# Kernel tuning notes

Measured on AMD Instinct MI355X. Metric: run time of the kernel, lower is better.

Reference implementation:

```python
import jax, jax.numpy as jnp
import numpy as np

N_NODES = 50000
N_EDGES = 600000
N_GRAPHS = 2048
EMB = 128
N_LAYERS = 3
ATOM_FEATS, ATOM_VOCAB = 9, 100
BOND_FEATS, BOND_VOCAB, BOND_DIM = 3, 8, 3


def setup_inputs() -> dict:
    key = jax.random.key(0)
    ks = jax.random.split(key, 10)
    x = jax.random.randint(ks[0], (N_NODES, ATOM_FEATS), 0, ATOM_VOCAB)
    edge_index = jax.random.randint(ks[1], (2, N_EDGES), 0, N_NODES)
    edge_attr = jax.random.randint(ks[2], (N_EDGES, BOND_FEATS), 0, BOND_VOCAB)
    batch = jnp.sort(jax.random.randint(ks[3], (N_NODES,), 0, N_GRAPHS))
    s = 1.0 / np.sqrt(EMB).astype(np.float32)
    atom_emb = jax.random.normal(ks[4], (ATOM_FEATS, ATOM_VOCAB, EMB), jnp.float32) * 0.1
    bond_emb = jax.random.normal(ks[5], (N_LAYERS, BOND_FEATS, BOND_VOCAB, BOND_DIM), jnp.float32) * 0.1
    W = jax.random.normal(ks[6], (N_LAYERS, BOND_DIM, EMB, EMB), jnp.float32) * s
    b = jnp.zeros((N_LAYERS, BOND_DIM, EMB), jnp.float32)
    fc1_w = jax.random.normal(ks[7], (EMB, EMB), jnp.float32) * s
    fc1_b = jnp.zeros((EMB,), jnp.float32)
    fc2_w = jax.random.normal(ks[8], (EMB, 1), jnp.float32) * s
    fc2_b = jnp.zeros((1,), jnp.float32)
    return dict(x=x, edge_index=edge_index, edge_attr=edge_attr, batch=batch,
                atom_emb=atom_emb, bond_emb=bond_emb, W=W, b=b,
                fc1_w=fc1_w, fc1_b=fc1_b, fc2_w=fc2_w, fc2_b=fc2_b)


def reference(x, edge_index, edge_attr, batch, atom_emb, bond_emb, W, b,
              fc1_w, fc1_b, fc2_w, fc2_b):
    src, dst = edge_index[0], edge_index[1]
    n = x.shape[0]
    # AtomEncoder: sum of per-column embedding lookups -> [N, EMB]
    h = atom_emb[0][x[:, 0]]
    for c in range(1, ATOM_FEATS):
        h = h + atom_emb[c][x[:, c]]
    for layer in range(N_LAYERS):
        # BondEncoder: [E, BOND_DIM] edge weights (one scalar channel per conv)
        ew = bond_emb[layer, 0][edge_attr[:, 0]]
        for c in range(1, BOND_FEATS):
            ew = ew + bond_emb[layer, c][edge_attr[:, c]]
        # Three parallel GCNConv(normalize=False): linear, gather src, edge-weight, scatter-add to dst
        msg = jnp.zeros((edge_index.shape[1], EMB), h.dtype)
        for k in range(BOND_DIM):
            xw = h @ W[layer, k]              # [N, EMB]
            msg = msg + ew[:, k:k + 1] * xw[src]   # [E, EMB]
        agg = jax.ops.segment_sum(msg, dst, num_segments=n)
        hn = agg + jnp.sum(b[layer], axis=0)  # sum of the three conv biases
        if layer < N_LAYERS - 1:
            hn = jax.nn.relu(hn)              # dropout is identity at eval
        h = hn + h                            # residual
    # global_mean_pool
    sums = jax.ops.segment_sum(h, batch, num_segments=N_GRAPHS)
    counts = jax.ops.segment_sum(jnp.ones((n,), h.dtype), batch, num_segments=N_GRAPHS)
    hg = sums / jnp.maximum(counts, 1.0)[:, None]
    return (hg @ fc1_w + fc1_b) @ fc2_w + fc2_b   # [N_GRAPHS, 1]
```

## Files before the change

### kernel.cpp

```cpp
#include <hip/hip_runtime.h>

#define N_NODES 50000
#define N_EDGES 600000
#define N_GRAPHS 2048
#define EMB 128
#define TDIM 384
#define TS_LD 392
#define HN (N_NODES * EMB)
#define GROWS 64

#define EPB 2048
#define NBLKA ((N_EDGES + EPB - 1) / EPB)
#define NCOARSE ((N_NODES + 255) / 256)
#define SCAN_TOT (NCOARSE * NBLKA)
#define SC2_NB ((SCAN_TOT + 255) / 256)

#define PRE_CNT_NB NBLKA
#define PRE_WCONV_NB 384
#define PRE_GB_NB 131

#define ATOM_HALF 25000
#define ATOM_NB 6250

typedef __attribute__((ext_vector_type(8))) short bf16x8;
typedef __attribute__((ext_vector_type(4))) float f32x4;
#define MFMA_BF16(a, b, c) __builtin_amdgcn_mfma_f32_16x16x32_bf16(a, b, c, 0, 0, 0)

#define AS1 __attribute__((address_space(1)))
#define AS3 __attribute__((address_space(3)))
__device__ inline void gl_lds16(const void* g, void* l) {
  __builtin_amdgcn_global_load_lds((const AS1 void*)g, (AS3 void*)l, 16, 0, 0);
}

__device__ inline unsigned short f2bf(float f) {
  unsigned int u = __float_as_uint(f);
  u += 0x7fffu + ((u >> 16) & 1u);
  return (unsigned short)(u >> 16);
}
__device__ inline float bf2f(unsigned short b) {
  return __uint_as_float(((unsigned int)b) << 16);
}
__device__ inline bf16x8 pack8(float4 lo, float4 hi) {
  bf16x8 r;
  r[0] = (short)f2bf(lo.x); r[1] = (short)f2bf(lo.y);
  r[2] = (short)f2bf(lo.z); r[3] = (short)f2bf(lo.w);
  r[4] = (short)f2bf(hi.x); r[5] = (short)f2bf(hi.y);
  r[6] = (short)f2bf(hi.z); r[7] = (short)f2bf(hi.w);
  return r;
}

__device__ inline void atom_block(int nbase, int blk, const int* __restrict__ x,
                                  const float* __restrict__ atom_emb,
                                  unsigned short* __restrict__ h_bf, float* sb) {
  const int wv = threadIdx.x >> 6;
  const int lane = threadIdx.x & 63;
  int n = nbase + blk * 4 + wv;
  if (n < N_NODES) {
    const int nu = __builtin_amdgcn_readfirstlane(n);
    const int* xr = x + nu * 9;
    int ix[9];
#pragma unroll
    for (int c = 0; c < 9; ++c) ix[c] = xr[c];
    float* wbase = sb + wv * 1280;
    const int half = lane >> 5;
    const int sub16 = lane & 31;
#pragma unroll
    for (int j = 0; j < 4; ++j) {
      int c = 2 * j + half;
      const float* g = atom_emb + (size_t)(c * 100 + ix[c]) * EMB + sub16 * 4;
      gl_lds16(g, wbase + j * 256);
    }
    {
      const float* g = atom_emb + (size_t)(8 * 100 + ix[8]) * EMB + sub16 * 4;
      gl_lds16(g, wbase + 1024);
    }
    asm volatile("s_waitcnt vmcnt(0)" ::: "memory");
    float2 acc = {0.f, 0.f};
#pragma unroll
    for (int c = 0; c < 9; ++c) {
      float2 v = *(const float2*)(wbase + c * 128 + lane * 2);
      acc.x += v.x; acc.y += v.y;
    }
    *(ushort2*)(h_bf + (size_t)nu * EMB + lane * 2) = ushort2{f2bf(acc.x), f2bf(acc.y)};
  }
}

__global__ __launch_bounds__(384) void k_pre(const int* __restrict__ ei,
                                             int* __restrict__ ghist,
                                             const float* __restrict__ W,
                                             unsigned short* __restrict__ wt,
                                             const int* __restrict__ batch,
                                             int* __restrict__ gs) {
  __shared__ int h[256];
  int blk = blockIdx.x;
  if (blk < PRE_CNT_NB) {
    const int t = threadIdx.x;
    if (t < 256) h[t] = 0;
    __syncthreads();
    const int base = blk * EPB;
#pragma unroll
    for (int k = 0; k < 6; ++k) {
      int o = k * 384 + t;
      int e = base + o;
      if (o < EPB && e < N_EDGES) atomicAdd(&h[ei[N_EDGES + e] >> 8], 1);
    }
    __syncthreads();
    if (t < NCOARSE) ghist[(size_t)t * NBLKA + blk] = h[t];
    return;
  }
  blk -= PRE_CNT_NB;
  if (blk < PRE_WCONV_NB) {
    int layer = blk >> 7, c = blk & 127, k = threadIdx.x;
    float v = W[(((layer * 3 + (k >> 7)) * 128) + (k & 127)) * 128 + c];
    wt[(size_t)blk * 384 + k] = f2bf(v);
    return;
  }
  blk -= PRE_WCONV_NB;
  {
    int i = blk * 384 + threadIdx.x;
    if (i < N_NODES) {
      int b = batch[i];
      int bp = (i == 0) ? -1 : batch[i - 1];
      for (int g = bp + 1; g <= b; ++g) gs[g] = i;
      if (i == N_NODES - 1) {
        for (int g = b + 1; g <= N_GRAPHS; ++g) gs[g] = N_NODES;
      }
    }
  }
}

__global__ __launch_bounds__(256) void k_gscan_a(int* __restrict__ ghist,
                                                 int* __restrict__ partials) {
  __shared__ int s[256];
  const int t = threadIdx.x;
  const int i = blockIdx.x * 256 + t;
  int v = (i < SCAN_TOT) ? ghist[i] : 0;
  s[t] = v;
  __syncthreads();
  for (int off = 1; off < 256; off <<= 1) {
    int u = (t >= off) ? s[t - off] : 0;
    __syncthreads();
    s[t] += u;
    __syncthreads();
  }
  if (i < SCAN_TOT) ghist[i] = s[t] - v;
  if (t == 255) partials[blockIdx.x] = s[255];
}

__global__ __launch_bounds__(256) void k_gscan_b(int* __restrict__ partials,
                                                 int* __restrict__ bucket_base,
                                                 int* __restrict__ row_start) {
  __shared__ int s[256];
  const int t = threadIdx.x;
  int v = (t < SC2_NB) ? partials[t] : 0;
  s[t] = v;
  __syncthreads();
  for (int off = 1; off < 256; off <<= 1) {
    int u = (t >= off) ? s[t - off] : 0;
    __syncthreads();
    s[t] += u;
    __syncthreads();
  }
  if (t < SC2_NB) partials[t] = s[t] - v;
  if (t == 0) { bucket_base[NCOARSE] = N_EDGES; row_start[N_NODES] = N_EDGES; }
}

__global__ __launch_bounds__(256) void k_gscan_c(int* __restrict__ ghist,
                                                 const int* __restrict__ partials,
                                                 int* __restrict__ bucket_base) {
  const int i = blockIdx.x * 256 + threadIdx.x;
  if (i < SCAN_TOT) {
    int g = ghist[i] + partials[blockIdx.x];
    ghist[i] = g;
    int d = i / NBLKA;
    if (i - d * NBLKA == 0) bucket_base[d] = g;
  }
}

__global__ __launch_bounds__(256) void k_coarse(const int* __restrict__ ei,
                                                const int* __restrict__ ea,
                                                const int* __restrict__ ghist,
                                                int2* __restrict__ tmp,
                                                const int* __restrict__ x,
                                                const float* __restrict__ atom_emb,
                                                unsigned short* __restrict__ h_bf) {
  __shared__ float sb[4 * 1280];
  if (blockIdx.x >= NBLKA) {
    atom_block(0, blockIdx.x - NBLKA, x, atom_emb, h_bf, sb);
    return;
  }
  int* cnt = (int*)sb;
  const int t = threadIdx.x;
  cnt[t] = 0;
  __syncthreads();
  const int base = blockIdx.x * EPB;
#pragma unroll
  for (int k = 0; k < 8; ++k) {
    int e = base + k * 256 + t;
    if (e < N_EDGES) {
      int dst = ei[N_EDGES + e];
      int d = dst >> 8;
      int r = atomicAdd(&cnt[d], 1);
      int pos = ghist[(size_t)d * NBLKA + blockIdx.x] + r;
      int eap = ea[e * 3 + 0] | (ea[e * 3 + 1] << 3) | (ea[e * 3 + 2] << 6);
      tmp[pos] = int2{dst | (eap << 16), ei[e]};
    }
  }
}

__global__ __launch_bounds__(256) void k_fine(const int2* __restrict__ tmp,
                                              const int* __restrict__ bucket_base,
                                              int* __restrict__ row_start,
                                              int2* __restrict__ sorted_se,
                                              const int* __restrict__ x,
                                              const float* __restrict__ atom_emb,
                                              unsigned short* __restrict__ h_bf) {
  __shared__ float sb[4 * 1280];
  if (blockIdx.x >= NCOARSE) {
    atom_block(ATOM_HALF, blockIdx.x - NCOARSE, x, atom_emb, h_bf, sb);
    return;
  }
  int* h = (int*)sb;
  int* s = h + 256;
  int* ex = s + 256;
  const int t = threadIdx.x;
  const int d = blockIdx.x;
  const int b0 = bucket_base[d], b1 = bucket_base[d + 1];
  h[t] = 0;
  __syncthreads();
  for (int i = b0 + t; i < b1; i += 256) atomicAdd(&h[tmp[i].x & 255], 1);
  __syncthreads();
  s[t] = h[t];
  __syncthreads();
  for (int off = 1; off < 256; off <<= 1) {
    int v = (t >= off) ? s[t - off] : 0;
    __syncthreads();
    s[t] += v;
    __syncthreads();
  }
  ex[t] = s[t] - h[t];
  int node = d * 256 + t;
  if (node < N_NODES) row_start[node] = b0 + ex[t];
  h[t] = 0;
  __syncthreads();
  for (int i = b0 + t; i < b1; i += 256) {
    int2 r = tmp[i];
    int f = r.x & 255;
    int pos = b0 + ex[f] + atomicAdd(&h[f], 1);
    sorted_se[pos] = int2{r.y, (r.x >> 16) & 511};
  }
}

__global__ __launch_bounds__(256) void k_agg(const int2* __restrict__ sorted_se,
                                             const int* __restrict__ row_start,
                                             const float* __restrict__ bl,
                                             const unsigned short* __restrict__ h_bf,
                                             unsigned short* __restrict__ t_bf) {
  __shared__ float4 combo[512];
  const int node = blockIdx.x * 16 + (threadIdx.x >> 4);
  const int sub = threadIdx.x & 15;
  const int beg = row_start[node], end = row_start[node + 1];
  int e = beg;
  const int full_end = beg + ((end - beg) & ~7);
  int2 se[8];
  if (e < full_end) {
#pragma unroll
    for (int j = 0; j < 8; ++j) se[j] = sorted_se[e + j];
  }
  for (int c = threadIdx.x; c < 512; c += 256) {
    int a0 = c & 7, a1 = (c >> 3) & 7, a2 = (c >> 6) & 7;
    combo[c] = float4{bl[a0 * 3 + 0] + bl[24 + a1 * 3 + 0] + bl[48 + a2 * 3 + 0],
                      bl[a0 * 3 + 1] + bl[24 + a1 * 3 + 1] + bl[48 + a2 * 3 + 1],
                      bl[a0 * 3 + 2] + bl[24 + a1 * 3 + 2] + bl[48 + a2 * 3 + 2], 0.f};
  }
  __syncthreads();
  float4 l0 = {0.f, 0.f, 0.f, 0.f}, h0 = l0;
  float4 l1 = l0, h1 = l0;
  float4 l2 = l0, h2 = l0;
  while (e < full_end) {
    bf16x8 u[8];
#pragma unroll
    for (int j = 0; j < 8; ++j)
      u[j] = *(const bf16x8*)(h_bf + (size_t)se[j].x * EMB + sub * 8);
    e += 8;
    int2 se_n[8];
    const bool more = (e < full_end);
    if (more) {
#pragma unroll
      for (int j = 0; j < 8; ++j) se_n[j] = sorted_se[e + j];
    }
#pragma unroll
    for (int j = 0; j < 8; ++j) {
      float4 w = combo[se[j].y];
      float4 vlo = {bf2f((unsigned short)u[j][0]), bf2f((unsigned short)u[j][1]),
                    bf2f((unsigned short)u[j][2]), bf2f((unsigned short)u[j][3])};
      float4 vhi = {bf2f((unsigned short)u[j][4]), bf2f((unsigned short)u[j][5]),
                    bf2f((unsigned short)u[j][6]), bf2f((unsigned short)u[j][7])};
      l0 += vlo * w.x; h0 += vhi * w.x;
      l1 += vlo * w.y; h1 += vhi * w.y;
      l2 += vlo * w.z; h2 += vhi * w.z;
    }
    if (more) {
#pragma unroll
      for (int j = 0; j < 8; ++j) se[j] = se_n[j];
    }
  }
  if (e < end) {
    int2 st[8];
#pragma unroll
    for (int j = 0; j < 8; ++j) {
      int idx = e + j;
      st[j] = sorted_se[idx < end ? idx : end - 1];
    }
    bf16x8 u[8];
#pragma unroll
    for (int j = 0; j < 8; ++j)
      u[j] = *(const bf16x8*)(h_bf + (size_t)st[j].x * EMB + sub * 8);
#pragma unroll
    for (int j = 0; j < 8; ++j) {
      float4 w = (e + j < end) ? combo[st[j].y] : float4{0.f, 0.f, 0.f, 0.f};
      float4 vlo = {bf2f((unsigned short)u[j][0]), bf2f((unsigned short)u[j][1]),
                    bf2f((unsigned short)u[j][2]), bf2f((unsigned short)u[j][3])};
      float4 vhi = {bf2f((unsigned short)u[j][4]), bf2f((unsigned short)u[j][5]),
                    bf2f((unsigned short)u[j][6]), bf2f((unsigned short)u[j][7])};
      l0 += vlo * w.x; h0 += vhi * w.x;
      l1 += vlo * w.y; h1 += vhi * w.y;
      l2 += vlo * w.z; h2 += vhi * w.z;
    }
  }
  size_t base = (size_t)node * TDIM + sub * 8;
  *(bf16x8*)(t_bf + base)       = pack8(l0, h0);
  *(bf16x8*)(t_bf + base + 128) = pack8(l1, h1);
  *(bf16x8*)(t_bf + base + 256) = pack8(l2, h2);
}

__global__ __launch_bounds__(512) void k_gemm(const unsigned short* __restrict__ t_bf,
                                              const unsigned short* __restrict__ wt,
                                              const float* __restrict__ bl,
                                              const unsigned short* __restrict__ h_in_bf,
                                              unsigned short* __restrict__ h_out_bf,
                                              int do_relu) {
  __shared__ unsigned short ts[GROWS * TS_LD];
  const int nb = blockIdx.x * GROWS;
  const int wv = threadIdx.x >> 6;
  const int lane = threadIdx.x & 63;
  const int m = lane & 15;
  const int kq = lane >> 4;
  const int c = wv * 16 + m;

  const unsigned short* pB = wt + (size_t)c * TDIM + kq * 8;
  bf16x8 B[12];
#pragma unroll
  for (int kc = 0; kc < 12; ++kc) B[kc] = *(const bf16x8*)(pB + kc * 32);
  const float bias = bl[c] + bl[128 + c] + bl[256 + c];

  for (int i = threadIdx.x; i < GROWS * 48; i += 512) {
    int r = i / 48, cc = i % 48;
    bf16x8 v = {};
    int row = nb + r;
    if (row < N_NODES) v = *(const bf16x8*)(t_bf + (size_t)row * TDIM + cc * 8);
    *(bf16x8*)(ts + r * TS_LD + cc * 8) = v;
  }
  __syncthreads();

#pragma unroll
  for (int rt = 0; rt < 4; ++rt) {
    const unsigned short* pA = ts + (rt * 16 + m) * TS_LD + kq * 8;
    bf16x8 A[12];
#pragma unroll
    for (int kc = 0; kc < 12; ++kc) A[kc] = *(const bf16x8*)(pA + kc * 32);
    f32x4 acc = {0.f, 0.f, 0.f, 0.f};
#pragma unroll
    for (int kc = 0; kc < 12; ++kc) acc = MFMA_BF16(A[kc], B[kc], acc);
#pragma unroll
    for (int r = 0; r < 4; ++r) {
      int row = nb + rt * 16 + kq * 4 + r;
      if (row < N_NODES) {
        size_t idx = (size_t)row * EMB + c;
        float v = acc[r] + bias;
        if (do_relu) v = fmaxf(v, 0.f);
        float hn = bf2f(h_in_bf[idx]) + v;
        h_out_bf[idx] = f2bf(hn);
      }
    }
  }
}

__global__ __launch_bounds__(128) void k_head(const unsigned short* __restrict__ h_bf,
                                              const int* __restrict__ gs,
                                              const float* __restrict__ fc1_w,
                                              const float* __restrict__ fc1_b,
                                              const float* __restrict__ fc2_w,
                                              const float* __restrict__ fc2_b,
                                              float* __restrict__ out) {
  __shared__ float hg[EMB];
  __shared__ float red[EMB];
  int g = blockIdx.x, e = threadIdx.x;
  int ns = gs[g], ne = gs[g + 1];
  float acc = 0.f;
  for (int n = ns; n < ne; ++n) acc += bf2f(h_bf[(size_t)n * EMB + e]);
  float cnt = fmaxf((float)(ne - ns), 1.f);
  hg[e] = acc / cnt;
  __syncthreads();
  float a2 = fc1_b[e];
  for (int j = 0; j < EMB; ++j) a2 += hg[j] * fc1_w[j * EMB + e];
  red[e] = a2 * fc2_w[e];
  __syncthreads();
  for (int s = 64; s > 0; s >>= 1) {
    if (e < s) red[e] += red[e + s];
    __syncthreads();
  }
  if (e == 0) out[g] = red[0] + fc2_b[0];
}

extern "C" void kernel_launch(void* const* d_in, const int* in_sizes, int n_in,
                              void* d_out, int out_size, void* d_ws, size_t ws_size,
                              hipStream_t stream) {
  const int*   x        = (const int*)d_in[0];
  const int*   ei       = (const int*)d_in[1];
  const int*   ea       = (const int*)d_in[2];
  const int*   batch    = (const int*)d_in[3];
  const float* atom_emb = (const float*)d_in[4];
  const float* bond_emb = (const float*)d_in[5];
  const float* W        = (const float*)d_in[6];
  const float* b        = (const float*)d_in[7];
  const float* fc1_w    = (const float*)d_in[8];
  const float* fc1_b    = (const float*)d_in[9];
  const float* fc2_w    = (const float*)d_in[10];
  const float* fc2_b    = (const float*)d_in[11];
  float* out = (float*)d_out;

  char* p = (char*)d_ws;
  auto alloc = [&](size_t bytes) { char* r = p; p += (bytes + 255) & ~(size_t)255; return r; };
  unsigned short* h0_bf      = (unsigned short*)alloc((size_t)HN * 2);
  unsigned short* h1_bf      = (unsigned short*)alloc((size_t)HN * 2);
  unsigned short* t_bf       = (unsigned short*)alloc((size_t)N_NODES * TDIM * 2);
  unsigned short* wt         = (unsigned short*)alloc((size_t)3 * 128 * TDIM * 2);
  int*            gs         = (int*)alloc((size_t)(N_GRAPHS + 1) * 4);
  int*            row_start  = (int*)alloc((size_t)(N_NODES + 1) * 4);
  int*            ghist      = (int*)alloc((size_t)SCAN_TOT * 4);
  int*            spart      = (int*)alloc((size_t)SC2_NB * 4);
  int*            bucket_base= (int*)alloc((size_t)(NCOARSE + 1) * 4);
  int2*           tmp_se     = (int2*)alloc((size_t)N_EDGES * 8);
  int2*           sorted_se  = (int2*)alloc((size_t)(N_EDGES + 8) * 8);

  const int pre_blocks = PRE_CNT_NB + PRE_WCONV_NB + PRE_GB_NB;
  k_pre<<<pre_blocks, 384, 0, stream>>>(ei, ghist, W, wt, batch, gs);
  k_gscan_a<<<SC2_NB, 256, 0, stream>>>(ghist, spart);
  k_gscan_b<<<1, 256, 0, stream>>>(spart, bucket_base, row_start);
  k_gscan_c<<<SC2_NB, 256, 0, stream>>>(ghist, spart, bucket_base);
  k_coarse<<<NBLKA + ATOM_NB, 256, 0, stream>>>(ei, ea, ghist, tmp_se,
                                                x, atom_emb, h0_bf);
  k_fine<<<NCOARSE + ATOM_NB, 256, 0, stream>>>(tmp_se, bucket_base, row_start, sorted_se,
                                                x, atom_emb, h0_bf);

  unsigned short* hib = h0_bf;
  unsigned short* hob = h1_bf;
  const int gemm_blocks = (N_NODES + GROWS - 1) / GROWS;
  for (int layer = 0; layer < 3; ++layer) {
    k_agg<<<N_NODES / 16, 256, 0, stream>>>(sorted_se, row_start, bond_emb + layer * 72,
                                            hib, t_bf);
    k_gemm<<<gemm_blocks, 512, 0, stream>>>(
        t_bf, wt + (size_t)layer * 128 * TDIM, b + layer * 3 * EMB,
        hib, hob, layer < 2 ? 1 : 0);
    unsigned short* tb = hib; hib = hob; hob = tb;
  }

  k_head<<<N_GRAPHS, 128, 0, stream>>>(hib, gs, fc1_w, fc1_b, fc2_w, fc2_b, out);
}
```

Before: 304.3 us.

## Fuse edge aggregation and GEMM into one per-layer kernel with LDS accumulation

Merges the aggregation kernel and the MFMA GEMM kernel into a single per-layer kernel, so the [N,384] bf16 intermediate tensor is no longer written to and read back from global memory. Each block takes 32 destination nodes and splits their edge range evenly across 32 groups of 16 threads for load balance. Each group accumulates partial sums in registers and flushes them into an fp32 LDS tile with atomicAdd whenever the destination node changes. The destination node index is now packed into the sorted edge record. The trade-off is LDS atomic traffic, a larger LDS footprint that may cut occupancy, and smaller 32-row GEMM tiles that reload the weight fragments more often.

```diff
diff --git a/kernel.cpp b/kernel.cpp
--- a/kernel.cpp
+++ b/kernel.cpp
@@ -7,7 +7,10 @@
 #define TDIM 384
 #define TS_LD 392
 #define HN (N_NODES * EMB)
-#define GROWS 64
+
+#define FN 32
+#define FGRID ((N_NODES + FN - 1) / FN)
+#define ACC_LD 388
 
 #define EPB 2048
 #define NBLKA ((N_EDGES + EPB - 1) / EPB)
@@ -39,14 +42,6 @@
 }
 __device__ inline float bf2f(unsigned short b) {
   return __uint_as_float(((unsigned int)b) << 16);
-}
-__device__ inline bf16x8 pack8(float4 lo, float4 hi) {
-  bf16x8 r;
-  r[0] = (short)f2bf(lo.x); r[1] = (short)f2bf(lo.y);
-  r[2] = (short)f2bf(lo.z); r[3] = (short)f2bf(lo.w);
-  r[4] = (short)f2bf(hi.x); r[5] = (short)f2bf(hi.y);
-  r[6] = (short)f2bf(hi.z); r[7] = (short)f2bf(hi.w);
-  return r;
 }
 
 __device__ inline void atom_block(int nbase, int blk, const int* __restrict__ x,
@@ -247,51 +242,83 @@
     int2 r = tmp[i];
     int f = r.x & 255;
     int pos = b0 + ex[f] + atomicAdd(&h[f], 1);
-    sorted_se[pos] = int2{r.y, (r.x >> 16) & 511};
-  }
-}
-
-__global__ __launch_bounds__(256) void k_agg(const int2* __restrict__ sorted_se,
-                                             const int* __restrict__ row_start,
-                                             const float* __restrict__ bl,
-                                             const unsigned short* __restrict__ h_bf,
-                                             unsigned short* __restrict__ t_bf) {
+    sorted_se[pos] = int2{r.y, ((r.x >> 16) & 511) | ((d * 256 + f) << 9)};
+  }
+}
+
+__device__ inline void flush24(float* a, float4& l0, float4& h0, float4& l1,
+                               float4& h1, float4& l2, float4& h2) {
+  atomicAdd(a + 0, l0.x); atomicAdd(a + 1, l0.y);
+  atomicAdd(a + 2, l0.z); atomicAdd(a + 3, l0.w);
+  atomicAdd(a + 4, h0.x); atomicAdd(a + 5, h0.y);
+  atomicAdd(a + 6, h0.z); atomicAdd(a + 7, h0.w);
+  atomicAdd(a + 128, l1.x); atomicAdd(a + 129, l1.y);
+  atomicAdd(a + 130, l1.z); atomicAdd(a + 131, l1.w);
+  atomicAdd(a + 132, h1.x); atomicAdd(a + 133, h1.y);
+  atomicAdd(a + 134, h1.z); atomicAdd(a + 135, h1.w);
+  atomicAdd(a + 256, l2.x); atomicAdd(a + 257, l2.y);
+  atomicAdd(a + 258, l2.z); atomicAdd(a + 259, l2.w);
+  atomicAdd(a + 260, h2.x); atomicAdd(a + 261, h2.y);
+  atomicAdd(a + 262, h2.z); atomicAdd(a + 263, h2.w);
+  float4 z = {0.f, 0.f, 0.f, 0.f};
+  l0 = z; h0 = z; l1 = z; h1 = z; l2 = z; h2 = z;
+}
+
+__global__ __launch_bounds__(512) void k_fused(const int2* __restrict__ sorted_se,
+                                               const int* __restrict__ row_start,
+                                               const float* __restrict__ bl,
+                                               const unsigned short* __restrict__ wt,
+                                               const float* __restrict__ bb,
+                                               const unsigned short* __restrict__ h_in_bf,
+                                               unsigned short* __restrict__ h_out_bf,
+                                               int do_relu) {
+  __shared__ float acc[FN * ACC_LD];
   __shared__ float4 combo[512];
-  const int node = blockIdx.x * 16 + (threadIdx.x >> 4);
-  const int sub = threadIdx.x & 15;
-  const int beg = row_start[node], end = row_start[node + 1];
-  int e = beg;
-  const int full_end = beg + ((end - beg) & ~7);
-  int2 se[8];
-  if (e < full_end) {
+  const int tid = threadIdx.x;
+  const int nb = blockIdx.x * FN;
+
+  {
+    int a0 = tid & 7, a1 = (tid >> 3) & 7, a2 = (tid >> 6) & 7;
+    combo[tid] = float4{bl[a0 * 3 + 0] + bl[24 + a1 * 3 + 0] + bl[48 + a2 * 3 + 0],
+                        bl[a0 * 3 + 1] + bl[24 + a1 * 3 + 1] + bl[48 + a2 * 3 + 1],
+                        bl[a0 * 3 + 2] + bl[24 + a1 * 3 + 2] + bl[48 + a2 * 3 + 2], 0.f};
+  }
+  for (int i = tid; i < FN * ACC_LD; i += 512) acc[i] = 0.f;
+  const int e0 = row_start[nb];
+  int ntop = nb + FN; if (ntop > N_NODES) ntop = N_NODES;
+  const int e1 = row_start[ntop];
+  __syncthreads();
+
+  const int qw = tid >> 4;
+  const int sub = tid & 15;
+  const int T = e1 - e0;
+  const int chunk = (T + 31) >> 5;
+  int cb = e0 + qw * chunk;
+  int ce = cb + chunk;
+  if (cb > e1) cb = e1;
+  if (ce > e1) ce = e1;
+
+  float4 l0 = {0.f, 0.f, 0.f, 0.f}, h0 = l0, l1 = l0, h1 = l0, l2 = l0, h2 = l0;
+  int cur = -1;
+  int e = cb;
+  const int full_end = cb + ((ce - cb) & ~7);
+  while (e < full_end) {
+    int2 se[8];
 #pragma unroll
     for (int j = 0; j < 8; ++j) se[j] = sorted_se[e + j];
-  }
-  for (int c = threadIdx.x; c < 512; c += 256) {
-    int a0 = c & 7, a1 = (c >> 3) & 7, a2 = (c >> 6) & 7;
-    combo[c] = float4{bl[a0 * 3 + 0] + bl[24 + a1 * 3 + 0] + bl[48 + a2 * 3 + 0],
-                      bl[a0 * 3 + 1] + bl[24 + a1 * 3 + 1] + bl[48 + a2 * 3 + 1],
-                      bl[a0 * 3 + 2] + bl[24 + a1 * 3 + 2] + bl[48 + a2 * 3 + 2], 0.f};
-  }
-  __syncthreads();
-  float4 l0 = {0.f, 0.f, 0.f, 0.f}, h0 = l0;
-  float4 l1 = l0, h1 = l0;
-  float4 l2 = l0, h2 = l0;
-  while (e < full_end) {
     bf16x8 u[8];
 #pragma unroll
     for (int j = 0; j < 8; ++j)
-      u[j] = *(const bf16x8*)(h_bf + (size_t)se[j].x * EMB + sub * 8);
-    e += 8;
-    int2 se_n[8];
-    const bool more = (e < full_end);
-    if (more) {
-#pragma unroll
-      for (int j = 0; j < 8; ++j) se_n[j] = sorted_se[e + j];
-    }
+      u[j] = *(const bf16x8*)(h_in_bf + (size_t)se[j].x * EMB + sub * 8);
 #pragma unroll
     for (int j = 0; j < 8; ++j) {
-      float4 w = combo[se[j].y];
+      int y = se[j].y;
+      int dl = (y >> 9) - nb;
+      if (dl != cur) {
+        if (cur >= 0) flush24(acc + cur * ACC_LD + sub * 8, l0, h0, l1, h1, l2, h2);
+        cur = dl;
+      }
+      float4 w = combo[y & 511];
       float4 vlo = {bf2f((unsigned short)u[j][0]), bf2f((unsigned short)u[j][1]),
                     bf2f((unsigned short)u[j][2]), bf2f((unsigned short)u[j][3])};
       float4 vhi = {bf2f((unsigned short)u[j][4]), bf2f((unsigned short)u[j][5]),
@@ -300,25 +327,28 @@
       l1 += vlo * w.y; h1 += vhi * w.y;
       l2 += vlo * w.z; h2 += vhi * w.z;
     }
-    if (more) {
-#pragma unroll
-      for (int j = 0; j < 8; ++j) se[j] = se_n[j];
-    }
-  }
-  if (e < end) {
-    int2 st[8];
+    e += 8;
+  }
+  if (e < ce) {
+    int2 se[8];
 #pragma unroll
     for (int j = 0; j < 8; ++j) {
       int idx = e + j;
-      st[j] = sorted_se[idx < end ? idx : end - 1];
+      se[j] = sorted_se[idx < ce ? idx : ce - 1];
     }
     bf16x8 u[8];
 #pragma unroll
     for (int j = 0; j < 8; ++j)
-      u[j] = *(const bf16x8*)(h_bf + (size_t)st[j].x * EMB + sub * 8);
+      u[j] = *(const bf16x8*)(h_in_bf + (size_t)se[j].x * EMB + sub * 8);
 #pragma unroll
     for (int j = 0; j < 8; ++j) {
-      float4 w = (e + j < end) ? combo[st[j].y] : float4{0.f, 0.f, 0.f, 0.f};
+      int y = se[j].y;
+      int dl = (y >> 9) - nb;
+      if (dl != cur) {
+        if (cur >= 0) flush24(acc + cur * ACC_LD + sub * 8, l0, h0, l1, h1, l2, h2);
+        cur = dl;
+      }
+      float4 w = (e + j < ce) ? combo[y & 511] : float4{0.f, 0.f, 0.f, 0.f};
       float4 vlo = {bf2f((unsigned short)u[j][0]), bf2f((unsigned short)u[j][1]),
                     bf2f((unsigned short)u[j][2]), bf2f((unsigned short)u[j][3])};
       float4 vhi = {bf2f((unsigned short)u[j][4]), bf2f((unsigned short)u[j][5]),
@@ -328,56 +358,53 @@
       l2 += vlo * w.z; h2 += vhi * w.z;
     }
   }
-  size_t base = (size_t)node * TDIM + sub * 8;
-  *(bf16x8*)(t_bf + base)       = pack8(l0, h0);
-  *(bf16x8*)(t_bf + base + 128) = pack8(l1, h1);
-  *(bf16x8*)(t_bf + base + 256) = pack8(l2, h2);
-}
-
-__global__ __launch_bounds__(512) void k_gemm(const unsigned short* __restrict__ t_bf,
-                                              const unsigned short* __restrict__ wt,
-                                              const float* __restrict__ bl,
-                                              const unsigned short* __restrict__ h_in_bf,
-                                              unsigned short* __restrict__ h_out_bf,
-                                              int do_relu) {
-  __shared__ unsigned short ts[GROWS * TS_LD];
-  const int nb = blockIdx.x * GROWS;
-  const int wv = threadIdx.x >> 6;
-  const int lane = threadIdx.x & 63;
+  if (cur >= 0) flush24(acc + cur * ACC_LD + sub * 8, l0, h0, l1, h1, l2, h2);
+  __syncthreads();
+
+  float vk[25];
+#pragma unroll
+  for (int k = 0; k < 25; ++k) {
+    int i = tid + k * 512;
+    vk[k] = (i < FN * ACC_LD) ? acc[i] : 0.f;
+  }
+  __syncthreads();
+  unsigned short* ts = (unsigned short*)acc;
+#pragma unroll
+  for (int k = 0; k < 25; ++k) {
+    int i = tid + k * 512;
+    if (i < FN * ACC_LD) {
+      int row = i / ACC_LD, col = i - row * ACC_LD;
+      if (col < TDIM) ts[row * TS_LD + col] = f2bf(vk[k]);
+    }
+  }
+  __syncthreads();
+
+  const int wv = tid >> 6;
+  const int lane = tid & 63;
   const int m = lane & 15;
   const int kq = lane >> 4;
   const int c = wv * 16 + m;
-
   const unsigned short* pB = wt + (size_t)c * TDIM + kq * 8;
   bf16x8 B[12];
 #pragma unroll
   for (int kc = 0; kc < 12; ++kc) B[kc] = *(const bf16x8*)(pB + kc * 32);
-  const float bias = bl[c] + bl[128 + c] + bl[256 + c];
-
-  for (int i = threadIdx.x; i < GROWS * 48; i += 512) {
-    int r = i / 48, cc = i % 48;
-    bf16x8 v = {};
-    int row = nb + r;
-    if (row < N_NODES) v = *(const bf16x8*)(t_bf + (size_t)row * TDIM + cc * 8);
-    *(bf16x8*)(ts + r * TS_LD + cc * 8) = v;
-  }
-  __syncthreads();
-
-#pragma unroll
-  for (int rt = 0; rt < 4; ++rt) {
+  const float bias = bb[c] + bb[128 + c] + bb[256 + c];
+
+#pragma unroll
+  for (int rt = 0; rt < 2; ++rt) {
     const unsigned short* pA = ts + (rt * 16 + m) * TS_LD + kq * 8;
     bf16x8 A[12];
 #pragma unroll
     for (int kc = 0; kc < 12; ++kc) A[kc] = *(const bf16x8*)(pA + kc * 32);
-    f32x4 acc = {0.f, 0.f, 0.f, 0.f};
-#pragma unroll
-    for (int kc = 0; kc < 12; ++kc) acc = MFMA_BF16(A[kc], B[kc], acc);
+    f32x4 ac = {0.f, 0.f, 0.f, 0.f};
+#pragma unroll
+    for (int kc = 0; kc < 12; ++kc) ac = MFMA_BF16(A[kc], B[kc], ac);
 #pragma unroll
     for (int r = 0; r < 4; ++r) {
       int row = nb + rt * 16 + kq * 4 + r;
       if (row < N_NODES) {
         size_t idx = (size_t)row * EMB + c;
-        float v = acc[r] + bias;
+        float v = ac[r] + bias;
         if (do_relu) v = fmaxf(v, 0.f);
         float hn = bf2f(h_in_bf[idx]) + v;
         h_out_bf[idx] = f2bf(hn);
@@ -434,7 +461,6 @@
   auto alloc = [&](size_t bytes) { char* r = p; p += (bytes + 255) & ~(size_t)255; return r; };
   unsigned short* h0_bf      = (unsigned short*)alloc((size_t)HN * 2);
   unsigned short* h1_bf      = (unsigned short*)alloc((size_t)HN * 2);
-  unsigned short* t_bf       = (unsigned short*)alloc((size_t)N_NODES * TDIM * 2);
   unsigned short* wt         = (unsigned short*)alloc((size_t)3 * 128 * TDIM * 2);
   int*            gs         = (int*)alloc((size_t)(N_GRAPHS + 1) * 4);
   int*            row_start  = (int*)alloc((size_t)(N_NODES + 1) * 4);
@@ -456,12 +482,10 @@
 
   unsigned short* hib = h0_bf;
   unsigned short* hob = h1_bf;
-  const int gemm_blocks = (N_NODES + GROWS - 1) / GROWS;
   for (int layer = 0; layer < 3; ++layer) {
-    k_agg<<<N_NODES / 16, 256, 0, stream>>>(sorted_se, row_start, bond_emb + layer * 72,
-                                            hib, t_bf);
-    k_gemm<<<gemm_blocks, 512, 0, stream>>>(
-        t_bf, wt + (size_t)layer * 128 * TDIM, b + layer * 3 * EMB,
+    k_fused<<<FGRID, 512, 0, stream>>>(
+        sorted_se, row_start, bond_emb + layer * 72,
+        wt + (size_t)layer * 128 * TDIM, b + layer * 3 * EMB,
         hib, hob, layer < 2 ? 1 : 0);
     unsigned short* tb = hib; hib = hob; hob = tb;
   }
```

Result: slower. 824.9 us (+171.1%).
